# Kernel tuning notes

Hardware: AMD Instinct MI355X
Metric: run time of the kernel (lower is better)

## Reference

```python
import jax, jax.numpy as jnp
import numpy as np

DIM = 4096
N_HEADS = 32
N_KV_HEADS = 8
HEAD_DIM = DIM // N_HEADS  # 128
SEQLEN = 2048
BATCH = 2
ROPE_THETA = 10000.0


def _precompute_freqs(seqlen, head_dim, theta):
    # matches torchtitan precompute_freqs_cis: freqs over even indices
    freqs = 1.0 / (theta ** (np.arange(0, head_dim, 2)[: head_dim // 2].astype(np.float32) / head_dim))
    t = np.arange(seqlen, dtype=np.float32)
    ang = np.outer(t, freqs)  # (S, head_dim//2)
    return jnp.asarray(np.cos(ang)), jnp.asarray(np.sin(ang))


def setup_inputs() -> dict:
    key = jax.random.key(0)
    kx, kq, kk, kv, ko = jax.random.split(key, 5)
    x = jax.random.normal(kx, (BATCH, SEQLEN, DIM), dtype=jnp.float32)
    wq = jax.random.normal(kq, (N_HEADS * HEAD_DIM, DIM), dtype=jnp.float32) * 0.02
    wk = jax.random.normal(kk, (N_KV_HEADS * HEAD_DIM, DIM), dtype=jnp.float32) * 0.02
    wv = jax.random.normal(kv, (N_KV_HEADS * HEAD_DIM, DIM), dtype=jnp.float32) * 0.02
    wo = jax.random.normal(ko, (DIM, N_HEADS * HEAD_DIM), dtype=jnp.float32) * 0.02
    cos, sin = _precompute_freqs(SEQLEN, HEAD_DIM, ROPE_THETA)
    return {"x": x, "cos": cos, "sin": sin, "wq": wq, "wk": wk, "wv": wv, "wo": wo}


def _apply_rope(t, cos, sin):
    # t: (B, S, H, hd); pairs (t[...,2i], t[...,2i+1]) rotated by angle
    tr = t.reshape(*t.shape[:-1], -1, 2)
    a, b = tr[..., 0], tr[..., 1]
    c = cos[None, :, None, :]  # (1, S, 1, hd//2)
    s = sin[None, :, None, :]
    out = jnp.stack([a * c - b * s, a * s + b * c], axis=-1)
    return out.reshape(t.shape)


def reference(x, cos, sin, wq, wk, wv, wo):
    B, S, D = x.shape
    hd = 2 * cos.shape[-1]
    H = wq.shape[0] // hd
    KVH = wk.shape[0] // hd
    n_rep = H // KVH

    q = (x @ wq.T).reshape(B, S, H, hd)
    k = (x @ wk.T).reshape(B, S, KVH, hd)
    v = (x @ wv.T).reshape(B, S, KVH, hd)

    q = _apply_rope(q, cos, sin)
    k = _apply_rope(k, cos, sin)

    # GQA: repeat_interleave kv heads (kept implicit via reshape of q into groups)
    qg = q.reshape(B, S, KVH, n_rep, hd)
    scale = 1.0 / jnp.sqrt(jnp.asarray(hd, dtype=x.dtype))
    # scores: (B, KVH, n_rep, S_q, S_k)
    scores = jnp.einsum("bsgrd,btgd->bgrst", qg, k) * scale
    causal = jnp.tril(jnp.ones((S, S), dtype=bool))
    scores = jnp.where(causal[None, None, None], scores, jnp.asarray(-1e30, dtype=scores.dtype))
    probs = jax.nn.softmax(scores, axis=-1)
    out = jnp.einsum("bgrst,btgd->bsgrd", probs, v).reshape(B, S, H * hd)
    return out @ wo.T
```

## Files before the change

kernel.cpp:

```cpp
#include <hip/hip_runtime.h>
#include <hip/hip_bf16.h>
#include <stdint.h>

#define DIM    4096
#define NH     32
#define NKVH   8
#define HD     128
#define SEQ    2048
#define BATCH  2
#define MTOT   (BATCH*SEQ)
#define SCALE  0.08838834764831845f

typedef __bf16 bf16_t;
typedef __bf16 bf16x8 __attribute__((ext_vector_type(8)));
typedef float  f32x4  __attribute__((ext_vector_type(4)));

#define AS1 __attribute__((address_space(1)))
#define AS3 __attribute__((address_space(3)))

__device__ __forceinline__ void gload_lds16(const void* g, void* l) {
    __builtin_amdgcn_global_load_lds((const AS1 void*)g, (AS3 void*)l, 16, 0, 0);
}

__device__ __forceinline__ void fence_barrier() {
    asm volatile("" ::: "memory");
    __builtin_amdgcn_s_barrier();
    asm volatile("" ::: "memory");
}

__global__ __launch_bounds__(256)
void cvt_f32_bf16(const float* __restrict__ in, bf16_t* __restrict__ out, int n4) {
    for (int i = blockIdx.x * blockDim.x + threadIdx.x; i < n4;
         i += gridDim.x * blockDim.x) {
        float4 v = reinterpret_cast<const float4*>(in)[i];
        union { bf16_t b[4]; uint2 u; } t;
        t.b[0] = (bf16_t)v.x; t.b[1] = (bf16_t)v.y;
        t.b[2] = (bf16_t)v.z; t.b[3] = (bf16_t)v.w;
        reinterpret_cast<uint2*>(out)[i] = t.u;
    }
}

__global__ __launch_bounds__(256)
void cvt_weights(const float* __restrict__ wq, const float* __restrict__ wk,
                 const float* __restrict__ wv, const float* __restrict__ wo,
                 bf16_t* __restrict__ out) {
    const int n0 = DIM * DIM / 4;
    const int n1 = NKVH * HD * DIM / 4;
    const int n2 = NKVH * HD * DIM / 4;
    const int n3 = DIM * DIM / 4;
    const int ntot = n0 + n1 + n2 + n3;
    for (int i = blockIdx.x * blockDim.x + threadIdx.x; i < ntot;
         i += gridDim.x * blockDim.x) {
        const float* src;
        int k = i;
        if (k < n0) src = wq;
        else if ((k -= n0) < n1) src = wk;
        else if ((k -= n1) < n2) src = wv;
        else { k -= n2; src = wo; }
        float4 v = reinterpret_cast<const float4*>(src)[k];
        union { bf16_t b[4]; uint2 u; } t;
        t.b[0] = (bf16_t)v.x; t.b[1] = (bf16_t)v.y;
        t.b[2] = (bf16_t)v.z; t.b[3] = (bf16_t)v.w;
        reinterpret_cast<uint2*>(out)[i] = t.u;
    }
}


__device__ __forceinline__ void stage_half(const bf16_t* gbase, int kt, int h,
                                           bf16_t* ldsdst, int tid, int w) {
#pragma unroll
    for (int t2 = 0; t2 < 2; ++t2) {
        int s = t2 * 512 + tid;
        int r = s >> 3, c = s & 7;
        gload_lds16(gbase + (size_t)(h * 128 + r) * DIM + kt + ((c ^ (r & 7)) * 8),
                    ldsdst + (size_t)(t2 * 512 + w * 64) * 8);
    }
}

__device__ __forceinline__ void read_a8(bf16x8* a, const bf16_t* Ahalf,
                                        int kk, int lr, int lg) {
#pragma unroll
    for (int mi = 0; mi < 8; ++mi) {
        int r = mi * 16 + lr;
        a[mi] = *(const bf16x8*)(Ahalf + r * 64 + ((kk * 4 + lg) ^ (r & 7)) * 8);
    }
}

__device__ __forceinline__ void read_b4(bf16x8* b, const bf16_t* Bhalf,
                                        int kk, int rb, int lg) {
#pragma unroll
    for (int ni = 0; ni < 4; ++ni) {
        int r = rb + ni * 16;
        b[ni] = *(const bf16x8*)(Bhalf + r * 64 + ((kk * 4 + lg) ^ (r & 7)) * 8);
    }
}

template<int MODE>
__global__ __launch_bounds__(512, 2)
void gemm8(const bf16_t* __restrict__ A,
           const bf16_t* __restrict__ B0,
           float* __restrict__ outF,
           bf16_t* __restrict__ outQ,
           bf16_t* __restrict__ outK,
           bf16_t* __restrict__ outV,
           const float* __restrict__ cosT,
           const float* __restrict__ sinT) {
    __shared__ __align__(16) bf16_t As[2][2][128 * 64];
    __shared__ __align__(16) bf16_t Bs[2][2][128 * 64];

    const int tid = threadIdx.x;
    const int l = tid & 63;
    const int w = tid >> 6;
    const int wm = w >> 2, wn = w & 3;
    const int lr = l & 15, lg = l >> 4;
    const int rb = (wn & 1) * 64 + lr;
    const int bh2 = wn >> 1;

    const int rowBase = blockIdx.x * 256;
    const int ct = blockIdx.y;

    const bf16_t* Ap = A + (size_t)rowBase * DIM;
    const bf16_t* Bp = B0 + (size_t)ct * 256 * DIM;

    f32x4 acc[8][4] = {};
    bf16x8 a0[8], a1[8], b0[4], b1[4];

    const int NT = DIM / 64;

    stage_half(Ap, 0,  0, &As[0][0][0], tid, w);
    stage_half(Ap, 0,  1, &As[0][1][0], tid, w);
    stage_half(Bp, 0,  0, &Bs[0][0][0], tid, w);
    stage_half(Bp, 0,  1, &Bs[0][1][0], tid, w);
    stage_half(Ap, 64, 0, &As[1][0][0], tid, w);
    stage_half(Ap, 64, 1, &As[1][1][0], tid, w);
    stage_half(Bp, 64, 0, &Bs[1][0][0], tid, w);
    stage_half(Bp, 64, 1, &Bs[1][1][0], tid, w);
    asm volatile("s_waitcnt vmcnt(8)" ::: "memory");
    fence_barrier();
    read_a8(a0, &As[0][wm][0], 0, lr, lg);
    read_b4(b0, &Bs[0][bh2][0], 0, rb, lg);

    for (int j = 0; j < NT; ++j) {
        const int buf = j & 1;
        const bf16_t* Ahalf = &As[buf][wm][0];
        const bf16_t* Bhalf = &Bs[buf][bh2][0];
        const int t2i = (j + 2 < NT) ? (j + 2) : (NT - 1);
        const int kt2 = t2i * 64;
        bf16_t* Adst = &As[t2i & 1][0][0];
        bf16_t* Bdst = &Bs[t2i & 1][0][0];

        read_a8(a1, Ahalf, 1, lr, lg);
        __builtin_amdgcn_s_setprio(1);
#pragma unroll
        for (int mi = 0; mi < 8; ++mi) {
            acc[mi][0] = __builtin_amdgcn_mfma_f32_16x16x32_bf16(a0[mi], b0[0], acc[mi][0], 0, 0, 0);
            acc[mi][1] = __builtin_amdgcn_mfma_f32_16x16x32_bf16(a0[mi], b0[1], acc[mi][1], 0, 0, 0);
        }
        __builtin_amdgcn_s_setprio(0);
        __builtin_amdgcn_sched_barrier(0);
        fence_barrier();

        read_b4(b1, Bhalf, 1, rb, lg);
        __builtin_amdgcn_s_setprio(1);
#pragma unroll
        for (int mi = 0; mi < 8; ++mi) {
            acc[mi][2] = __builtin_amdgcn_mfma_f32_16x16x32_bf16(a0[mi], b0[2], acc[mi][2], 0, 0, 0);
            acc[mi][3] = __builtin_amdgcn_mfma_f32_16x16x32_bf16(a0[mi], b0[3], acc[mi][3], 0, 0, 0);
        }
        __builtin_amdgcn_s_setprio(0);
        __builtin_amdgcn_sched_barrier(0);
        asm volatile("s_waitcnt lgkmcnt(0)" ::: "memory");
        fence_barrier();

        stage_half(Ap, kt2, 0, Adst, tid, w);
        stage_half(Ap, kt2, 1, Adst + 128 * 64, tid, w);
        __builtin_amdgcn_s_setprio(1);
#pragma unroll
        for (int mi = 0; mi < 8; ++mi) {
            acc[mi][0] = __builtin_amdgcn_mfma_f32_16x16x32_bf16(a1[mi], b1[0], acc[mi][0], 0, 0, 0);
            acc[mi][1] = __builtin_amdgcn_mfma_f32_16x16x32_bf16(a1[mi], b1[1], acc[mi][1], 0, 0, 0);
        }
        __builtin_amdgcn_s_setprio(0);
        __builtin_amdgcn_sched_barrier(0);
        fence_barrier();

        stage_half(Bp, kt2, 0, Bdst, tid, w);
        stage_half(Bp, kt2, 1, Bdst + 128 * 64, tid, w);
        __builtin_amdgcn_s_setprio(1);
#pragma unroll
        for (int mi = 0; mi < 8; ++mi) {
            acc[mi][2] = __builtin_amdgcn_mfma_f32_16x16x32_bf16(a1[mi], b1[2], acc[mi][2], 0, 0, 0);
            acc[mi][3] = __builtin_amdgcn_mfma_f32_16x16x32_bf16(a1[mi], b1[3], acc[mi][3], 0, 0, 0);
        }
        __builtin_amdgcn_s_setprio(0);
        __builtin_amdgcn_sched_barrier(0);
        asm volatile("s_waitcnt vmcnt(8)" ::: "memory");
        fence_barrier();
        if (j + 1 < NT) {
            read_a8(a0, &As[buf ^ 1][wm][0], 0, lr, lg);
            read_b4(b0, &Bs[buf ^ 1][bh2][0], 0, rb, lg);
        }
    }

#pragma unroll
    for (int mi = 0; mi < 8; ++mi) {
        int gmBase = rowBase + wm * 128 + mi * 16 + lg * 4;
#pragma unroll
        for (int ni = 0; ni < 4; ++ni) {
            f32x4 v4 = acc[mi][ni];
            int gn = ct * 256 + wn * 64 + ni * 16 + lr;
            if (MODE == 0) {
#pragma unroll
                for (int i = 0; i < 4; ++i)
                    outF[(size_t)(gmBase + i) * DIM + gn] = v4[i];
            } else {
                if (ct < 16) {
                    int h = gn >> 7, d = gn & 127, pi2 = d >> 1;
#pragma unroll
                    for (int i = 0; i < 4; ++i) {
                        float v = v4[i];
                        float pvv = __shfl_xor(v, 1);
                        int gm = gmBase + i;
                        int bb = gm >> 11, sidx = gm & (SEQ - 1);
                        float c = cosT[sidx * 64 + pi2], sn = sinT[sidx * 64 + pi2];
                        float o = (d & 1) ? (pvv * sn + v * c) : (v * c - pvv * sn);
                        outQ[((size_t)(bb * NH + h) * SEQ + sidx) * HD + d] = (bf16_t)o;
                    }
                } else if (ct < 20) {
                    int kn = gn - 4096;
                    int h = kn >> 7, d = kn & 127, pi2 = d >> 1;
#pragma unroll
                    for (int i = 0; i < 4; ++i) {
                        float v = v4[i];
                        float pvv = __shfl_xor(v, 1);
                        int gm = gmBase + i;
                        int bb = gm >> 11, sidx = gm & (SEQ - 1);
                        float c = cosT[sidx * 64 + pi2], sn = sinT[sidx * 64 + pi2];
                        float o = (d & 1) ? (pvv * sn + v * c) : (v * c - pvv * sn);
                        outK[((size_t)(bb * NKVH + h) * SEQ + sidx) * HD + d] = (bf16_t)o;
                    }
                } else {
                    int vn = gn - 5120;
                    int kvh = vn >> 7, d = vn & 127;
#pragma unroll
                    for (int i = 0; i < 4; ++i) {
                        float dummy = __shfl_xor(v4[i], 1); (void)dummy;
                        int gm = gmBase + i;
                        int bb = gm >> 11, sidx = gm & (SEQ - 1);
                        outV[((size_t)(bb * NKVH + kvh) * HD + d) * SEQ + sidx] = (bf16_t)v4[i];
                    }
                }
            }
        }
    }
}

__global__ __launch_bounds__(256, 2)
void attn_fwd(const bf16_t* __restrict__ Qr,
              const bf16_t* __restrict__ Kr,
              const bf16_t* __restrict__ Vt,
              bf16_t* __restrict__ Ob) {
    __shared__ __align__(16) bf16_t Ks[2][64 * 128];
    __shared__ __align__(16) bf16_t Vs[2][128 * 64];
    __shared__ __align__(16) bf16_t Ps[4][32 * 64];

    const int tid = threadIdx.x;
    const int l  = tid & 63;
    const int w  = tid >> 6;
    const int lr = l & 15, lg = l >> 4;
    const int e  = lr & 7;

    const int qt  = 15 - (blockIdx.x >> 6);
    const int bh  = blockIdx.x & 63;
    const int b   = bh >> 5;
    const int h   = bh & 31;
    const int kvh = h >> 2;
    const int q0  = qt * 128;
    const int nt  = 2 * qt + 2;
    const int qmin = q0 + w * 32;

    const bf16_t* kbase = Kr + (size_t)(b * NKVH + kvh) * SEQ * HD;
    const bf16_t* vbase = Vt + (size_t)(b * NKVH + kvh) * HD * SEQ;

    bf16x8 qf[2][4];
    const bf16_t* qp = Qr + ((size_t)(b * NH + h) * SEQ + qmin + lr) * HD;
#pragma unroll
    for (int mi = 0; mi < 2; ++mi)
#pragma unroll
        for (int kk = 0; kk < 4; ++kk)
            qf[mi][kk] = *(const bf16x8*)(qp + (size_t)mi * 16 * HD + kk * 32 + lg * 8);

    f32x4 oacc[2][8] = {};
    float mrow[2] = {-1e30f, -1e30f};
    float lsum[2] = {0.f, 0.f};

#pragma unroll
    for (int t2 = 0; t2 < 4; ++t2) {
        int s = t2 * 256 + tid;
        { int r = s >> 4, g = (s & 15) ^ (r & 7);
          gload_lds16(kbase + (size_t)r * HD + g * 8,
                      &Ks[0][(size_t)(t2 * 256 + w * 64) * 8]); }
        { int r = s >> 3, g = (s & 7) ^ (r & 7);
          gload_lds16(vbase + (size_t)r * SEQ + g * 8,
                      &Vs[0][(size_t)(t2 * 256 + w * 64) * 8]); }
    }
    __syncthreads();

    int cur = 0;
    for (int t = 0; t < nt; ++t) {
        if (t + 1 < nt) {
            const int kv1 = (t + 1) * 64;
#pragma unroll
            for (int t2 = 0; t2 < 4; ++t2) {
                int s = t2 * 256 + tid;
                { int r = s >> 4, g = (s & 15) ^ (r & 7);
                  gload_lds16(kbase + (size_t)(kv1 + r) * HD + g * 8,
                              &Ks[cur ^ 1][(size_t)(t2 * 256 + w * 64) * 8]); }
                { int r = s >> 3, g = (s & 7) ^ (r & 7);
                  gload_lds16(vbase + (size_t)r * SEQ + kv1 + g * 8,
                              &Vs[cur ^ 1][(size_t)(t2 * 256 + w * 64) * 8]); }
            }
        }

        const bool active = (t * 64) <= (qmin + 31);
        if (active) {
            const bool needMask = (t * 64 + 63) > qmin;

            f32x4 sf[2][4] = {};
#pragma unroll
            for (int kk = 0; kk < 4; ++kk)
#pragma unroll
                for (int nf = 0; nf < 4; ++nf) {
                    bf16x8 kf = *(const bf16x8*)(
                        &Ks[cur][(nf * 16 + lr) * 128 + ((kk * 4 + lg) ^ e) * 8]);
#pragma unroll
                    for (int mi = 0; mi < 2; ++mi)
                        sf[mi][nf] = __builtin_amdgcn_mfma_f32_16x16x32_bf16(
                            kf, qf[mi][kk], sf[mi][nf], 0, 0, 0);
                }

            float aO[2][4];
#pragma unroll
            for (int mi = 0; mi < 2; ++mi) {
                const int qrow = qmin + mi * 16 + lr;
                float mt = -1e30f;
#pragma unroll
                for (int nf = 0; nf < 4; ++nf)
#pragma unroll
                    for (int i = 0; i < 4; ++i) {
                        float sc = sf[mi][nf][i] * SCALE;
                        if (needMask && (t * 64 + nf * 16 + lg * 4 + i) > qrow)
                            sc = -1e30f;
                        sf[mi][nf][i] = sc;
                        mt = fmaxf(mt, sc);
                    }
                mt = fmaxf(mt, __shfl_xor(mt, 16));
                mt = fmaxf(mt, __shfl_xor(mt, 32));
                float mnew = fmaxf(mrow[mi], mt);
                float alpha = __expf(mrow[mi] - mnew);
                mrow[mi] = mnew;
                float rs = 0.f;
#pragma unroll
                for (int nf = 0; nf < 4; ++nf)
#pragma unroll
                    for (int i = 0; i < 4; ++i) {
                        float p = __expf(sf[mi][nf][i] - mnew);
                        sf[mi][nf][i] = p;
                        rs += p;
                    }
                rs += __shfl_xor(rs, 16);
                rs += __shfl_xor(rs, 32);
                lsum[mi] = lsum[mi] * alpha + rs;
#pragma unroll
                for (int i = 0; i < 4; ++i)
                    aO[mi][i] = __shfl(alpha, lg * 4 + i);
            }

#pragma unroll
            for (int mi = 0; mi < 2; ++mi)
#pragma unroll
                for (int df = 0; df < 8; ++df)
#pragma unroll
                    for (int i = 0; i < 4; ++i)
                        oacc[mi][df][i] *= aO[mi][i];

#pragma unroll
            for (int mi = 0; mi < 2; ++mi)
#pragma unroll
                for (int nf = 0; nf < 4; ++nf) {
                    union { bf16_t bb[4]; uint2 u; } pk;
#pragma unroll
                    for (int i = 0; i < 4; ++i) pk.bb[i] = (bf16_t)sf[mi][nf][i];
                    int addr = (mi * 16 + lr) * 64 +
                               (((nf * 2 + (lg >> 1)) ^ e) << 3) + (lg & 1) * 4;
                    *(uint2*)(&Ps[w][addr]) = pk.u;
                }
            asm volatile("s_waitcnt lgkmcnt(0)" ::: "memory");
            __builtin_amdgcn_sched_barrier(0);

            bf16x8 pf[2][2];
#pragma unroll
            for (int mi = 0; mi < 2; ++mi)
#pragma unroll
                for (int k2 = 0; k2 < 2; ++k2)
                    pf[mi][k2] = *(const bf16x8*)(
                        &Ps[w][(mi * 16 + lr) * 64 + ((k2 * 4 + lg) ^ e) * 8]);
#pragma unroll
            for (int df = 0; df < 8; ++df)
#pragma unroll
                for (int k2 = 0; k2 < 2; ++k2) {
                    bf16x8 vf = *(const bf16x8*)(
                        &Vs[cur][(df * 16 + lr) * 64 + ((k2 * 4 + lg) ^ e) * 8]);
#pragma unroll
                    for (int mi = 0; mi < 2; ++mi)
                        oacc[mi][df] = __builtin_amdgcn_mfma_f32_16x16x32_bf16(
                            pf[mi][k2], vf, oacc[mi][df], 0, 0, 0);
                }
        }
        __syncthreads();
        cur ^= 1;
    }

#pragma unroll
    for (int mi = 0; mi < 2; ++mi) {
        float ls[4];
#pragma unroll
        for (int i = 0; i < 4; ++i)
            ls[i] = 1.f / __shfl(lsum[mi], lg * 4 + i);
#pragma unroll
        for (int df = 0; df < 8; ++df)
#pragma unroll
            for (int i = 0; i < 4; ++i) {
                float o = oacc[mi][df][i] * ls[i];
                int gm = b * SEQ + qmin + mi * 16 + lg * 4 + i;
                int gn = h * HD + df * 16 + lr;
                Ob[(size_t)gm * DIM + gn] = (bf16_t)o;
            }
    }
}

extern "C" void kernel_launch(void* const* d_in, const int* in_sizes, int n_in,
                              void* d_out, int out_size, void* d_ws, size_t ws_size,
                              hipStream_t stream) {
    const float* x    = (const float*)d_in[0];
    const float* cosT = (const float*)d_in[1];
    const float* sinT = (const float*)d_in[2];
    const float* wq   = (const float*)d_in[3];
    const float* wk   = (const float*)d_in[4];
    const float* wv   = (const float*)d_in[5];
    const float* wo   = (const float*)d_in[6];

    bf16_t* p = (bf16_t*)d_ws;
    bf16_t* xb  = p; p += (size_t)MTOT * DIM;
    bf16_t* wb  = p; p += (size_t)(DIM + 2 * NKVH * HD + DIM) * DIM;
    bf16_t* Qr  = p; p += (size_t)MTOT * DIM;
    bf16_t* Kr  = p; p += (size_t)BATCH * NKVH * SEQ * HD;
    bf16_t* Vt  = p; p += (size_t)BATCH * NKVH * HD * SEQ;
    bf16_t* Ob  = p; p += (size_t)MTOT * DIM;

    bf16_t* wob = wb + (size_t)(DIM + 2 * NKVH * HD) * DIM;

    cvt_f32_bf16<<<2048, 256, 0, stream>>>(x, xb, MTOT * DIM / 4);
    cvt_weights<<<2048, 256, 0, stream>>>(wq, wk, wv, wo, wb);

    gemm8<3><<<dim3(16, 24), 512, 0, stream>>>(
        xb, wb, nullptr, Qr, Kr, Vt, cosT, sinT);

    attn_fwd<<<1024, 256, 0, stream>>>(Qr, Kr, Vt, Ob);

    gemm8<0><<<dim3(16, 16), 512, 0, stream>>>(
        Ob, wob, (float*)d_out, nullptr, nullptr, nullptr, nullptr, nullptr);
}
```

Before: 526.2 us.

## Restructure GEMM main loop into quarter-tile phases with staggered A/B prefetch

```diff
diff --git a/kernel.cpp b/kernel.cpp
--- a/kernel.cpp
+++ b/kernel.cpp
@@ -77,21 +77,25 @@
     }
 }
 
-__device__ __forceinline__ void read_a8(bf16x8* a, const bf16_t* Ahalf,
-                                        int kk, int lr, int lg) {
-#pragma unroll
-    for (int mi = 0; mi < 8; ++mi) {
-        int r = mi * 16 + lr;
-        a[mi] = *(const bf16x8*)(Ahalf + r * 64 + ((kk * 4 + lg) ^ (r & 7)) * 8);
-    }
-}
-
-__device__ __forceinline__ void read_b4(bf16x8* b, const bf16_t* Bhalf,
-                                        int kk, int rb, int lg) {
-#pragma unroll
-    for (int ni = 0; ni < 4; ++ni) {
-        int r = rb + ni * 16;
-        b[ni] = *(const bf16x8*)(Bhalf + r * 64 + ((kk * 4 + lg) ^ (r & 7)) * 8);
+__device__ __forceinline__ void read_a4(bf16x8 a[4][2], const bf16_t* Ahalf,
+                                        int mh, int lr, int lg) {
+#pragma unroll
+    for (int mi = 0; mi < 4; ++mi) {
+        int r = mh * 64 + mi * 16 + lr;
+#pragma unroll
+        for (int kk = 0; kk < 2; ++kk)
+            a[mi][kk] = *(const bf16x8*)(Ahalf + r * 64 + ((kk * 4 + lg) ^ (r & 7)) * 8);
+    }
+}
+
+__device__ __forceinline__ void read_b2(bf16x8 b[2][2], const bf16_t* Bhalf,
+                                        int np, int rb, int lg) {
+#pragma unroll
+    for (int ni = 0; ni < 2; ++ni) {
+        int r = rb + (np * 2 + ni) * 16;
+#pragma unroll
+        for (int kk = 0; kk < 2; ++kk)
+            b[ni][kk] = *(const bf16x8*)(Bhalf + r * 64 + ((kk * 4 + lg) ^ (r & 7)) * 8);
     }
 }
 
@@ -114,92 +118,101 @@
     const int wm = w >> 2, wn = w & 3;
     const int lr = l & 15, lg = l >> 4;
     const int rb = (wn & 1) * 64 + lr;
-    const int bh2 = wn >> 1;
-
-    const int rowBase = blockIdx.x * 256;
-    const int ct = blockIdx.y;
+
+    constexpr int NY = (MODE == 3) ? 24 : 16;
+    const int nwg = 16 * NY;
+    const int bid = blockIdx.y * gridDim.x + blockIdx.x;
+    const int swz = (bid & 7) * (nwg >> 3) + (bid >> 3);
+    const int bx = swz / NY;
+    const int ct = swz - bx * NY;
+    const int rowBase = bx * 256;
 
     const bf16_t* Ap = A + (size_t)rowBase * DIM;
     const bf16_t* Bp = B0 + (size_t)ct * 256 * DIM;
 
     f32x4 acc[8][4] = {};
-    bf16x8 a0[8], a1[8], b0[4], b1[4];
+    bf16x8 aq[4][2];
+    bf16x8 bA[2][2];
+    bf16x8 bB[2][2];
 
     const int NT = DIM / 64;
 
+    stage_half(Bp, 0,  0, &Bs[0][0][0], tid, w);
+    stage_half(Bp, 0,  1, &Bs[0][1][0], tid, w);
     stage_half(Ap, 0,  0, &As[0][0][0], tid, w);
     stage_half(Ap, 0,  1, &As[0][1][0], tid, w);
-    stage_half(Bp, 0,  0, &Bs[0][0][0], tid, w);
-    stage_half(Bp, 0,  1, &Bs[0][1][0], tid, w);
-    stage_half(Ap, 64, 0, &As[1][0][0], tid, w);
-    stage_half(Ap, 64, 1, &As[1][1][0], tid, w);
     stage_half(Bp, 64, 0, &Bs[1][0][0], tid, w);
     stage_half(Bp, 64, 1, &Bs[1][1][0], tid, w);
-    asm volatile("s_waitcnt vmcnt(8)" ::: "memory");
+    asm volatile("s_waitcnt vmcnt(4)" ::: "memory");
     fence_barrier();
-    read_a8(a0, &As[0][wm][0], 0, lr, lg);
-    read_b4(b0, &Bs[0][bh2][0], 0, rb, lg);
 
     for (int j = 0; j < NT; ++j) {
-        const int buf = j & 1;
-        const bf16_t* Ahalf = &As[buf][wm][0];
-        const bf16_t* Bhalf = &Bs[buf][bh2][0];
-        const int t2i = (j + 2 < NT) ? (j + 2) : (NT - 1);
-        const int kt2 = t2i * 64;
-        bf16_t* Adst = &As[t2i & 1][0][0];
-        bf16_t* Bdst = &Bs[t2i & 1][0][0];
-
-        read_a8(a1, Ahalf, 1, lr, lg);
+        const int s = j & 1;
+        const bf16_t* Ah = &As[s][wm][0];
+        const bf16_t* Bh = &Bs[s][wn >> 1][0];
+        const int ktA = ((j + 1 < NT) ? j + 1 : NT - 1) * 64;
+        const int ktB = ((j + 2 < NT) ? j + 2 : NT - 1) * 64;
+
+        read_a4(aq, Ah, 0, lr, lg);
+        read_b2(bA, Bh, 0, rb, lg);
+        stage_half(Ap, ktA, 0, &As[s ^ 1][0][0], tid, w);
+        asm volatile("s_waitcnt lgkmcnt(8)" ::: "memory");
+        fence_barrier();
+        asm volatile("s_waitcnt lgkmcnt(0)" ::: "memory");
         __builtin_amdgcn_s_setprio(1);
 #pragma unroll
-        for (int mi = 0; mi < 8; ++mi) {
-            acc[mi][0] = __builtin_amdgcn_mfma_f32_16x16x32_bf16(a0[mi], b0[0], acc[mi][0], 0, 0, 0);
-            acc[mi][1] = __builtin_amdgcn_mfma_f32_16x16x32_bf16(a0[mi], b0[1], acc[mi][1], 0, 0, 0);
-        }
+        for (int kk = 0; kk < 2; ++kk)
+#pragma unroll
+            for (int mi = 0; mi < 4; ++mi) {
+                acc[mi][0] = __builtin_amdgcn_mfma_f32_16x16x32_bf16(aq[mi][kk], bA[0][kk], acc[mi][0], 0, 0, 0);
+                acc[mi][1] = __builtin_amdgcn_mfma_f32_16x16x32_bf16(aq[mi][kk], bA[1][kk], acc[mi][1], 0, 0, 0);
+            }
         __builtin_amdgcn_s_setprio(0);
-        __builtin_amdgcn_sched_barrier(0);
-        fence_barrier();
-
-        read_b4(b1, Bhalf, 1, rb, lg);
+        fence_barrier();
+
+        read_b2(bB, Bh, 1, rb, lg);
+        stage_half(Ap, ktA, 1, &As[s ^ 1][1][0], tid, w);
+        fence_barrier();
+        asm volatile("s_waitcnt lgkmcnt(0)" ::: "memory");
         __builtin_amdgcn_s_setprio(1);
 #pragma unroll
-        for (int mi = 0; mi < 8; ++mi) {
-            acc[mi][2] = __builtin_amdgcn_mfma_f32_16x16x32_bf16(a0[mi], b0[2], acc[mi][2], 0, 0, 0);
-            acc[mi][3] = __builtin_amdgcn_mfma_f32_16x16x32_bf16(a0[mi], b0[3], acc[mi][3], 0, 0, 0);
-        }
+        for (int kk = 0; kk < 2; ++kk)
+#pragma unroll
+            for (int mi = 0; mi < 4; ++mi) {
+                acc[mi][2] = __builtin_amdgcn_mfma_f32_16x16x32_bf16(aq[mi][kk], bB[0][kk], acc[mi][2], 0, 0, 0);
+                acc[mi][3] = __builtin_amdgcn_mfma_f32_16x16x32_bf16(aq[mi][kk], bB[1][kk], acc[mi][3], 0, 0, 0);
+            }
         __builtin_amdgcn_s_setprio(0);
-        __builtin_amdgcn_sched_barrier(0);
+        fence_barrier();
+
+        read_a4(aq, Ah, 1, lr, lg);
+        stage_half(Bp, ktB, 0, &Bs[s][0][0], tid, w);
+        fence_barrier();
         asm volatile("s_waitcnt lgkmcnt(0)" ::: "memory");
-        fence_barrier();
-
-        stage_half(Ap, kt2, 0, Adst, tid, w);
-        stage_half(Ap, kt2, 1, Adst + 128 * 64, tid, w);
         __builtin_amdgcn_s_setprio(1);
 #pragma unroll
-        for (int mi = 0; mi < 8; ++mi) {
-            acc[mi][0] = __builtin_amdgcn_mfma_f32_16x16x32_bf16(a1[mi], b1[0], acc[mi][0], 0, 0, 0);
-            acc[mi][1] = __builtin_amdgcn_mfma_f32_16x16x32_bf16(a1[mi], b1[1], acc[mi][1], 0, 0, 0);
-        }
+        for (int kk = 0; kk < 2; ++kk)
+#pragma unroll
+            for (int mi = 0; mi < 4; ++mi) {
+                acc[mi + 4][0] = __builtin_amdgcn_mfma_f32_16x16x32_bf16(aq[mi][kk], bA[0][kk], acc[mi + 4][0], 0, 0, 0);
+                acc[mi + 4][1] = __builtin_amdgcn_mfma_f32_16x16x32_bf16(aq[mi][kk], bA[1][kk], acc[mi + 4][1], 0, 0, 0);
+            }
         __builtin_amdgcn_s_setprio(0);
-        __builtin_amdgcn_sched_barrier(0);
-        fence_barrier();
-
-        stage_half(Bp, kt2, 0, Bdst, tid, w);
-        stage_half(Bp, kt2, 1, Bdst + 128 * 64, tid, w);
+        fence_barrier();
+
+        stage_half(Bp, ktB, 1, &Bs[s][1][0], tid, w);
+        fence_barrier();
         __builtin_amdgcn_s_setprio(1);
 #pragma unroll
-        for (int mi = 0; mi < 8; ++mi) {
-            acc[mi][2] = __builtin_amdgcn_mfma_f32_16x16x32_bf16(a1[mi], b1[2], acc[mi][2], 0, 0, 0);
-            acc[mi][3] = __builtin_amdgcn_mfma_f32_16x16x32_bf16(a1[mi], b1[3], acc[mi][3], 0, 0, 0);
-        }
+        for (int kk = 0; kk < 2; ++kk)
+#pragma unroll
+            for (int mi = 0; mi < 4; ++mi) {
+                acc[mi + 4][2] = __builtin_amdgcn_mfma_f32_16x16x32_bf16(aq[mi][kk], bB[0][kk], acc[mi + 4][2], 0, 0, 0);
+                acc[mi + 4][3] = __builtin_amdgcn_mfma_f32_16x16x32_bf16(aq[mi][kk], bB[1][kk], acc[mi + 4][3], 0, 0, 0);
+            }
         __builtin_amdgcn_s_setprio(0);
-        __builtin_amdgcn_sched_barrier(0);
-        asm volatile("s_waitcnt vmcnt(8)" ::: "memory");
-        fence_barrier();
-        if (j + 1 < NT) {
-            read_a8(a0, &As[buf ^ 1][wm][0], 0, lr, lg);
-            read_b4(b0, &Bs[buf ^ 1][bh2][0], 0, rb, lg);
-        }
+        asm volatile("s_waitcnt vmcnt(4)" ::: "memory");
+        fence_barrier();
     }
 
 #pragma unroll
```

Result: slower. 576.1 us (+9.5%).
